# Optimization experiments

Hardware: AMD Instinct MI355X
Metric: run time of the kernel (lower is better)

## Reference

```python
import jax, jax.numpy as jnp
import numpy as np

B, T, D = 64, 256, 512   # batch, seq_len, input_dim (= emb_dim)
HA = 512                 # alpha_dim
HB = 512                 # beta_dim (must equal alpha_dim due to source bug)
ODE = 256                # ode_dim


def _lin(key, out_d, in_d, scale):
    k1, k2 = jax.random.split(key)
    W = jax.random.uniform(k1, (out_d, in_d), jnp.float32, -scale, scale)
    b = jax.random.uniform(k2, (out_d,), jnp.float32, -scale, scale)
    return W, b


def setup_inputs() -> dict:
    key = jax.random.key(0)
    ks = jax.random.split(key, 16)
    x = jax.random.normal(ks[0], (B, T, D), jnp.float32)
    W_emb, b_emb = _lin(ks[1], D, D, 1.0 / np.sqrt(D))
    # LSTMCell params: gates order i, f, g, o ; shapes (4H, in) / (4H, H)
    sA = 1.0 / np.sqrt(HA)
    Wih_a = jax.random.uniform(ks[2], (4 * HA, D), jnp.float32, -sA, sA)
    Whh_a = jax.random.uniform(ks[3], (4 * HA, HA), jnp.float32, -sA, sA)
    bih_a = jax.random.uniform(ks[4], (4 * HA,), jnp.float32, -sA, sA)
    bhh_a = jax.random.uniform(ks[5], (4 * HA,), jnp.float32, -sA, sA)
    sB = 1.0 / np.sqrt(HB)
    Wih_b = jax.random.uniform(ks[6], (4 * HB, D), jnp.float32, -sB, sB)
    Whh_b = jax.random.uniform(ks[7], (4 * HB, HB), jnp.float32, -sB, sB)
    bih_b = jax.random.uniform(ks[8], (4 * HB,), jnp.float32, -sB, sB)
    bhh_b = jax.random.uniform(ks[9], (4 * HB,), jnp.float32, -sB, sB)
    W_aatt, b_aatt = _lin(ks[10], 1, HA, 1.0 / np.sqrt(HA))
    W_batt, b_batt = _lin(ks[11], D, HB, 1.0 / np.sqrt(HB))
    W_mu, b_mu = _lin(ks[12], ODE, D, 1.0 / np.sqrt(D))
    W_sig, b_sig = _lin(ks[13], ODE, D, 1.0 / np.sqrt(D))
    ah0 = jax.random.normal(ks[14], (B, HA), jnp.float32)
    k15a, k15b, k15c = jax.random.split(ks[15], 3)
    ac0 = jax.random.normal(k15a, (B, HA), jnp.float32)
    bh0 = jax.random.normal(k15b, (B, HB), jnp.float32)
    bc0 = jax.random.normal(k15c, (B, HB), jnp.float32)
    return dict(x=x, W_emb=W_emb, b_emb=b_emb,
                Wih_a=Wih_a, Whh_a=Whh_a, bih_a=bih_a, bhh_a=bhh_a,
                Wih_b=Wih_b, Whh_b=Whh_b, bih_b=bih_b, bhh_b=bhh_b,
                W_aatt=W_aatt, b_aatt=b_aatt, W_batt=W_batt, b_batt=b_batt,
                W_mu=W_mu, b_mu=b_mu, W_sig=W_sig, b_sig=b_sig,
                ah0=ah0, ac0=ac0, bh0=bh0, bc0=bc0)


def _lstm_scan(xs, h0, c0, Wih, Whh, bih, bhh):
    # xs: (T, B, D) -> (hs (T,B,H), hT (B,H))
    def step(carry, xt):
        h, c = carry
        g = xt @ Wih.T + bih + h @ Whh.T + bhh
        i, f, gg, o = jnp.split(g, 4, axis=-1)
        c = jax.nn.sigmoid(f) * c + jax.nn.sigmoid(i) * jnp.tanh(gg)
        h = jax.nn.sigmoid(o) * jnp.tanh(c)
        return (h, c), h
    (hT, _), hs = jax.lax.scan(step, (h0, c0), xs)
    return hs, hT


def reference(x, W_emb, b_emb, Wih_a, Whh_a, bih_a, bhh_a,
              Wih_b, Whh_b, bih_b, bhh_b, W_aatt, b_aatt,
              W_batt, b_batt, W_mu, b_mu, W_sig, b_sig,
              ah0, ac0, bh0, bc0):
    emb = x @ W_emb.T + b_emb                      # (B, T, D)
    rev = jnp.flip(emb.transpose(1, 0, 2), 0)      # (T, B, D) reversed time
    hs_a, hT_a = _lstm_scan(rev, ah0, ac0, Wih_a, Whh_a, bih_a, bhh_a)
    hi = jnp.flip(hs_a, 0).transpose(1, 0, 2)      # (B, T, HA)
    alpha = jax.nn.softmax(hi @ W_aatt.T + b_aatt, axis=1)  # (B, T, 1)
    # Faithful to source bug: beta loop appends the FINAL alpha_hx each step,
    # so gi is hT_a broadcast over time (beta LSTM output is discarded).
    _ = _lstm_scan(rev, bh0, bc0, Wih_b, Whh_b, bih_b, bhh_b)  # dead compute, DCE'd
    gi = jnp.broadcast_to(hT_a[:, None, :], (x.shape[0], x.shape[1], hT_a.shape[-1]))
    beta = jnp.tanh(gi @ W_batt.T + b_batt)        # (B, T, D)
    w = alpha * beta * emb                          # (B, T, D)
    var = jnp.sum(w, axis=1)                        # (B, D)
    mean = jnp.mean(w, axis=1)                      # (B, D)
    mu = mean @ W_mu.T + b_mu                       # (B, ODE)
    sigma = var @ W_sig.T + b_sig                   # (B, ODE)
    return (mu, sigma)
```

## Files before the change

kernel.cpp:

```cpp
#include <hip/hip_runtime.h>
#include <hip/hip_bf16.h>
#include <math.h>

#define BB_ 64
#define TT_ 256
#define DD_ 512
#define HH_ 512
#define G4_ 2048
#define ODE_ 256

#define NBLK_ 256

__device__ __forceinline__ float2 cohload2(const float* p) {
    unsigned long long u = __hip_atomic_load(
        (unsigned long long*)p, __ATOMIC_RELAXED, __HIP_MEMORY_SCOPE_AGENT);
    union { unsigned long long u; float2 f; } c; c.u = u;
    return c.f;
}
__device__ __forceinline__ void cohstore2(float* p, float a, float b) {
    union { unsigned long long u; float2 f; } c; c.f = make_float2(a, b);
    __hip_atomic_store((unsigned long long*)p, c.u,
                       __ATOMIC_RELAXED, __HIP_MEMORY_SCOPE_AGENT);
}

__device__ __forceinline__ float fsigmoid(float x) {
    return 1.f / (1.f + __expf(-x));
}
__device__ __forceinline__ float ftanh(float x) {
    float e = __expf(-2.f * fabsf(x));
    float t = (1.f - e) / (1.f + e);
    return copysignf(t, x);
}

template <int CTRL>
__device__ __forceinline__ float dpp_ror_add(float x) {
    int y = __builtin_amdgcn_update_dpp(0, __float_as_int(x), CTRL, 0xf, 0xf, false);
    return x + __int_as_float(y);
}
__device__ __forceinline__ float row16_allreduce(float x) {
    x = dpp_ror_add<0x121>(x);
    x = dpp_ror_add<0x122>(x);
    x = dpp_ror_add<0x124>(x);
    x = dpp_ror_add<0x128>(x);
    return x;
}

template <int ACT>
__global__ __launch_bounds__(256) void gemm_bt(
    const float* __restrict__ A, const float* __restrict__ W,
    const float* __restrict__ bias1, const float* __restrict__ bias2,
    float* __restrict__ C, int M, int N, int K, float scale)
{
    const int BM = 128, BN = 128, BK = 16;
    __shared__ float As[BK][BM + 4];
    __shared__ float Ws[BK][BN + 4];
    const int tid = threadIdx.x;
    const int tx = tid & 15, ty = tid >> 4;
    const int m0 = blockIdx.y * BM, n0 = blockIdx.x * BN;

    float acc[8][8];
#pragma unroll
    for (int i = 0; i < 8; ++i)
#pragma unroll
        for (int j = 0; j < 8; ++j) acc[i][j] = 0.f;

    for (int k0 = 0; k0 < K; k0 += BK) {
#pragma unroll
        for (int i = 0; i < 2; ++i) {
            int lin = (i * 256 + tid) * 4;
            int r = lin >> 4, c = lin & 15;
            int gm = m0 + r; if (gm > M - 1) gm = M - 1;
            float4 av = *(const float4*)(A + (size_t)gm * K + k0 + c);
            As[c + 0][r] = av.x; As[c + 1][r] = av.y;
            As[c + 2][r] = av.z; As[c + 3][r] = av.w;
            float4 wv = *(const float4*)(W + (size_t)(n0 + r) * K + k0 + c);
            Ws[c + 0][r] = wv.x; Ws[c + 1][r] = wv.y;
            Ws[c + 2][r] = wv.z; Ws[c + 3][r] = wv.w;
        }
        __syncthreads();
#pragma unroll
        for (int k = 0; k < BK; ++k) {
            float a[8], w[8];
#pragma unroll
            for (int i = 0; i < 8; ++i) a[i] = As[k][ty * 8 + i];
#pragma unroll
            for (int j = 0; j < 8; ++j) w[j] = Ws[k][tx * 8 + j];
#pragma unroll
            for (int i = 0; i < 8; ++i)
#pragma unroll
                for (int j = 0; j < 8; ++j) acc[i][j] += a[i] * w[j];
        }
        __syncthreads();
    }

#pragma unroll
    for (int j = 0; j < 8; ++j) {
        int n = n0 + tx * 8 + j;
        float bsum = bias1[n] + (bias2 ? bias2[n] : 0.f);
#pragma unroll
        for (int i = 0; i < 8; ++i) {
            int m = m0 + ty * 8 + i;
            if (m < M) {
                float v = acc[i][j] * scale + bsum;
                if (ACT == 1) v = tanhf(v);
                C[(size_t)m * N + n] = v;
            }
        }
    }
}

__global__ __launch_bounds__(256) void lstm_persist(
    const float* __restrict__ gx,
    const float* __restrict__ Whh,
    const float* __restrict__ ac0,
    float* __restrict__ hT0,
    float* __restrict__ hT1,
    float* __restrict__ hsT,
    unsigned* __restrict__ cnt)
{
    __shared__ float h_s[512 * 20];
    __shared__ float gx_s[8 * 65];

    const int tid = threadIdx.x;
    const int jb = blockIdx.x >> 3;
    const int bg = blockIdx.x & 7;
    const int jh0 = jb * 16;
    const int b0  = bg * 8;
    const int kq   = tid & 15;
    const int jh_l = tid >> 4;
    const int jh   = jh0 + jh_l;

    float creg = 0.f;
    if (kq < 8) creg = ac0[(size_t)(b0 + kq) * HH_ + jh];

    float4 wreg[32];
#pragma unroll
    for (int kk = 0; kk < 32; ++kk) {
        int k = kk * 16 + kq;
        wreg[kk].x = Whh[(size_t)(0 * 512 + jh) * 512 + k];
        wreg[kk].y = Whh[(size_t)(1 * 512 + jh) * 512 + k];
        wreg[kk].z = Whh[(size_t)(2 * 512 + jh) * 512 + k];
        wreg[kk].w = Whh[(size_t)(3 * 512 + jh) * 512 + k];
    }

    const int g_lb  = tid >> 5;
    const int g_g   = (tid >> 3) & 3;
    const int g_jl2 = (tid & 7) * 2;
    const float* gsrc = gx + (size_t)(b0 + g_lb) * TT_ * G4_ + g_g * 512 + jh0 + g_jl2;

    float2 gxreg = *(const float2*)(gsrc + (size_t)255 * G4_);

    for (int t = 0; t < TT_; ++t) {
        const float* hin = ((t & 1) ? hT1 : hT0) + (size_t)bg * 4096;
        float* hout      = ((t & 1) ? hT0 : hT1) + (size_t)bg * 4096;

        gx_s[g_lb * 65 + g_g * 16 + g_jl2]     = gxreg.x;
        gx_s[g_lb * 65 + g_g * 16 + g_jl2 + 1] = gxreg.y;

        float4 hstg[4];
#pragma unroll
        for (int w = 0; w < 4; ++w) {
            int c = w * 256 + tid;
            float2 a  = cohload2(hin + (size_t)c * 4);
            float2 b2 = cohload2(hin + (size_t)c * 4 + 2);
            hstg[w] = make_float4(a.x, a.y, b2.x, b2.y);
        }
#pragma unroll
        for (int w = 0; w < 4; ++w) {
            int c = w * 256 + tid;
            *(float4*)(h_s + (c >> 1) * 20 + (c & 1) * 4) = hstg[w];
        }
        __syncthreads();

        if (t + 1 < TT_)
            gxreg = *(const float2*)(gsrc + (size_t)(TT_ - 2 - t) * G4_);

        float acc[8][4];
#pragma unroll
        for (int i = 0; i < 8; ++i)
#pragma unroll
            for (int j = 0; j < 4; ++j) acc[i][j] = 0.f;

#pragma unroll
        for (int kk = 0; kk < 32; ++kk) {
            int k = kk * 16 + kq;
            float4 wv = wreg[kk];
            float4 ha = *(const float4*)(h_s + (size_t)k * 20);
            float4 hb = *(const float4*)(h_s + (size_t)k * 20 + 4);
            float hv[8] = {ha.x, ha.y, ha.z, ha.w, hb.x, hb.y, hb.z, hb.w};
#pragma unroll
            for (int bb = 0; bb < 8; ++bb) {
                acc[bb][0] += hv[bb] * wv.x;
                acc[bb][1] += hv[bb] * wv.y;
                acc[bb][2] += hv[bb] * wv.z;
                acc[bb][3] += hv[bb] * wv.w;
            }
        }

#pragma unroll
        for (int bb = 0; bb < 8; ++bb)
#pragma unroll
            for (int g = 0; g < 4; ++g)
                acc[bb][g] = row16_allreduce(acc[bb][g]);

        float hn = 0.f;
        if (kq < 8) {
            float gi = 0.f, gf = 0.f, gg = 0.f, go = 0.f;
#pragma unroll
            for (int bb = 0; bb < 8; ++bb)
                if (kq == bb) { gi = acc[bb][0]; gf = acc[bb][1];
                                gg = acc[bb][2]; go = acc[bb][3]; }
            gi += gx_s[kq * 65 + 0 * 16 + jh_l];
            gf += gx_s[kq * 65 + 1 * 16 + jh_l];
            gg += gx_s[kq * 65 + 2 * 16 + jh_l];
            go += gx_s[kq * 65 + 3 * 16 + jh_l];
            float si = fsigmoid(gi);
            float sf = fsigmoid(gf);
            float sg = ftanh(gg);
            float so = fsigmoid(go);
            creg = sf * creg + si * sg;
            hn = so * ftanh(creg);
        }
        float hn_up = __shfl_down(hn, 1);
        const bool do_st = (kq < 8) && ((kq & 1) == 0);
        if (do_st)
            cohstore2(hout + (size_t)jh * 8 + kq, hn, hn_up);

        __syncthreads();
        if (tid == 0)
            __hip_atomic_fetch_add(&cnt[(size_t)bg * 32], 1u,
                                   __ATOMIC_RELAXED, __HIP_MEMORY_SCOPE_AGENT);
        if (do_st)
            *(float2*)(hsT + ((size_t)t * 512 + jh) * 64 + b0 + kq) = make_float2(hn, hn_up);
        if (tid == 0) {
            unsigned tgt = (unsigned)(t + 1) * 32u;
            while (__hip_atomic_load(&cnt[(size_t)bg * 32],
                        __ATOMIC_RELAXED, __HIP_MEMORY_SCOPE_AGENT) < tgt)
                __builtin_amdgcn_s_sleep(1);
        }
        __syncthreads();
    }
}

__global__ __launch_bounds__(256) void h0_transpose(
    const float* __restrict__ ah0, float* __restrict__ hT0)
{
    int idx = blockIdx.x * 256 + threadIdx.x;
    int b = idx >> 9, jh = idx & 511;
    hT0[(size_t)(b >> 3) * 4096 + jh * 8 + (b & 7)] = ah0[idx];
}

__global__ __launch_bounds__(256) void att_scores_T(
    const float* __restrict__ hsT, const float* __restrict__ Wa,
    const float* __restrict__ ba, float* __restrict__ scores)
{
    int ts = blockIdx.x;
    int b = threadIdx.x & 63, part = threadIdx.x >> 6;
    const float* hp = hsT + (size_t)ts * 512 * 64;
    float s = 0.f;
#pragma unroll 8
    for (int jj = 0; jj < 128; ++jj) {
        int jh = part * 128 + jj;
        s += hp[(size_t)jh * 64 + b] * Wa[jh];
    }
    __shared__ float red[4][64];
    red[part][b] = s;
    __syncthreads();
    if (part == 0) {
        float tot = red[0][b] + red[1][b] + red[2][b] + red[3][b] + ba[0];
        scores[b * TT_ + (TT_ - 1 - ts)] = tot;
    }
}

__global__ __launch_bounds__(256) void softmax_wsum(
    const float* __restrict__ scores, const float* __restrict__ emb,
    float* __restrict__ s)
{
    const int b = blockIdx.x;
    const int tid = threadIdx.x;
    __shared__ float sm[256];
    __shared__ float red[16];
    float v = scores[b * TT_ + tid];
    float m = v;
#pragma unroll
    for (int off = 32; off; off >>= 1) m = fmaxf(m, __shfl_xor(m, off));
    int wv = tid >> 6, ln = tid & 63;
    if (ln == 0) red[wv] = m;
    __syncthreads();
    float bm = fmaxf(fmaxf(red[0], red[1]), fmaxf(red[2], red[3]));
    float e = expf(v - bm);
    float ss = e;
#pragma unroll
    for (int off = 32; off; off >>= 1) ss += __shfl_xor(ss, off);
    if (ln == 0) red[8 + wv] = ss;
    __syncthreads();
    float tot = red[8] + red[9] + red[10] + red[11];
    sm[tid] = e / tot;
    __syncthreads();

    float acc0 = 0.f, acc1 = 0.f;
    const float* ep = emb + (size_t)b * TT_ * DD_;
    for (int t = 0; t < TT_; ++t) {
        float a = sm[t];
        acc0 += a * ep[t * DD_ + tid];
        acc1 += a * ep[t * DD_ + 256 + tid];
    }
    s[b * DD_ + tid] = acc0;
    s[b * DD_ + 256 + tid] = acc1;
}

__global__ __launch_bounds__(256) void beta_from_hT(
    const float* __restrict__ hTT, const float* __restrict__ Wb,
    const float* __restrict__ bbias, float* __restrict__ beta)
{
    int b = threadIdx.x & 63, w = threadIdx.x >> 6;
    int d = blockIdx.x * 4 + w;
    const float* wrow = Wb + (size_t)d * 512;
    const float* hb = hTT + (size_t)(b >> 3) * 4096 + (b & 7);
    float s = 0.f;
#pragma unroll 8
    for (int jh = 0; jh < 512; ++jh)
        s += hb[(size_t)jh * 8] * wrow[jh];
    beta[(size_t)b * 512 + d] = tanhf(s + bbias[d]);
}

__global__ __launch_bounds__(256) void mulvec(
    const float* __restrict__ a, const float* __restrict__ b,
    float* __restrict__ o, int n)
{
    int i = blockIdx.x * 256 + threadIdx.x;
    if (i < n) o[i] = a[i] * b[i];
}

extern "C" void kernel_launch(void* const* d_in, const int* in_sizes, int n_in,
                              void* d_out, int out_size, void* d_ws, size_t ws_size,
                              hipStream_t stream) {
    const float* x      = (const float*)d_in[0];
    const float* W_emb  = (const float*)d_in[1];
    const float* b_emb  = (const float*)d_in[2];
    const float* Wih_a  = (const float*)d_in[3];
    const float* Whh_a  = (const float*)d_in[4];
    const float* bih_a  = (const float*)d_in[5];
    const float* bhh_a  = (const float*)d_in[6];
    const float* W_aatt = (const float*)d_in[11];
    const float* b_aatt = (const float*)d_in[12];
    const float* W_batt = (const float*)d_in[13];
    const float* b_batt = (const float*)d_in[14];
    const float* W_mu   = (const float*)d_in[15];
    const float* b_mu   = (const float*)d_in[16];
    const float* W_sig  = (const float*)d_in[17];
    const float* b_sig  = (const float*)d_in[18];
    const float* ah0    = (const float*)d_in[19];
    const float* ac0    = (const float*)d_in[20];

    const size_t N_EMB = (size_t)BB_ * TT_ * DD_;
    const size_t N_GX  = (size_t)BB_ * TT_ * G4_;
    const size_t N_HS  = (size_t)TT_ * HH_ * BB_;
    const size_t N_BH  = (size_t)BB_ * HH_;
    const size_t N_BAR = 8192;

    size_t need_floats = N_BAR + N_EMB + N_GX + N_HS + 2 * N_BH
                       + (size_t)BB_ * TT_ + 3 * N_BH;
    if (ws_size < need_floats * sizeof(float)) return;

    float* ws     = (float*)d_ws;
    unsigned* cnt = (unsigned*)d_ws;
    float* emb    = ws + N_BAR;
    float* gx     = emb + N_EMB;
    float* hsT    = gx + N_GX;
    float* hT0    = hsT + N_HS;
    float* hT1    = hT0 + N_BH;
    float* scores = hT1 + N_BH;
    float* svec   = scores + (size_t)BB_ * TT_;
    float* beta   = svec + N_BH;
    float* var    = beta + N_BH;

    float* out_mu  = (float*)d_out;
    float* out_sig = out_mu + (size_t)BB_ * ODE_;

    hipMemsetAsync(d_ws, 0, N_BAR * sizeof(float), stream);

    h0_transpose<<<dim3(128), dim3(256), 0, stream>>>(ah0, hT0);

    gemm_bt<0><<<dim3(DD_ / 128, (BB_ * TT_) / 128), dim3(256), 0, stream>>>(
        x, W_emb, b_emb, nullptr, emb, BB_ * TT_, DD_, DD_, 1.f);

    gemm_bt<0><<<dim3(G4_ / 128, (BB_ * TT_) / 128), dim3(256), 0, stream>>>(
        emb, Wih_a, bih_a, bhh_a, gx, BB_ * TT_, G4_, DD_, 1.f);

    lstm_persist<<<dim3(NBLK_), dim3(256), 0, stream>>>(
        gx, Whh_a, ac0, hT0, hT1, hsT, cnt);

    att_scores_T<<<dim3(TT_), dim3(256), 0, stream>>>(hsT, W_aatt, b_aatt, scores);

    softmax_wsum<<<dim3(BB_), dim3(256), 0, stream>>>(scores, emb, svec);

    beta_from_hT<<<dim3(DD_ / 4), dim3(256), 0, stream>>>(hT0, W_batt, b_batt, beta);

    mulvec<<<dim3(N_BH / 256), dim3(256), 0, stream>>>(beta, svec, var, (int)N_BH);

    gemm_bt<0><<<dim3(ODE_ / 128, 1), dim3(256), 0, stream>>>(
        var, W_mu, b_mu, nullptr, out_mu, BB_, ODE_, DD_, 1.f / 256.f);
    gemm_bt<0><<<dim3(ODE_ / 128, 1), dim3(256), 0, stream>>>(
        var, W_sig, b_sig, nullptr, out_sig, BB_, ODE_, DD_, 1.f);
}
```

Measured before the change: 1.782 ms.

## Replace block-level barriers with per-wavefront counters in recurrent LSTM sync

The inter-block step barrier is rewritten so each wavefront signals its own counter slot after draining its stores, and every wavefront polls the four per-wave counters of its batch group itself. This removes two __syncthreads per timestep and the single-thread serialisation of the grid barrier. In exchange it relies on s_waitcnt ordering rather than block barriers for visibility of h stores, and the counter array is now four times larger. The last step skips the barrier entirely.

```diff
diff --git a/kernel.cpp b/kernel.cpp
--- a/kernel.cpp
+++ b/kernel.cpp
@@ -129,6 +129,8 @@
     const int kq   = tid & 15;
     const int jh_l = tid >> 4;
     const int jh   = jh0 + jh_l;
+    const int wv   = tid >> 6;
+    const int ln   = tid & 63;
 
     float creg = 0.f;
     if (kq < 8) creg = ac0[(size_t)(b0 + kq) * HH_ + jh];
@@ -184,16 +186,16 @@
 #pragma unroll
         for (int kk = 0; kk < 32; ++kk) {
             int k = kk * 16 + kq;
-            float4 wv = wreg[kk];
+            float4 wvv = wreg[kk];
             float4 ha = *(const float4*)(h_s + (size_t)k * 20);
             float4 hb = *(const float4*)(h_s + (size_t)k * 20 + 4);
             float hv[8] = {ha.x, ha.y, ha.z, ha.w, hb.x, hb.y, hb.z, hb.w};
 #pragma unroll
             for (int bb = 0; bb < 8; ++bb) {
-                acc[bb][0] += hv[bb] * wv.x;
-                acc[bb][1] += hv[bb] * wv.y;
-                acc[bb][2] += hv[bb] * wv.z;
-                acc[bb][3] += hv[bb] * wv.w;
+                acc[bb][0] += hv[bb] * wvv.x;
+                acc[bb][1] += hv[bb] * wvv.y;
+                acc[bb][2] += hv[bb] * wvv.z;
+                acc[bb][3] += hv[bb] * wvv.w;
             }
         }
 
@@ -226,19 +228,29 @@
         if (do_st)
             cohstore2(hout + (size_t)jh * 8 + kq, hn, hn_up);
 
-        __syncthreads();
-        if (tid == 0)
-            __hip_atomic_fetch_add(&cnt[(size_t)bg * 32], 1u,
-                                   __ATOMIC_RELAXED, __HIP_MEMORY_SCOPE_AGENT);
-        if (do_st)
-            *(float2*)(hsT + ((size_t)t * 512 + jh) * 64 + b0 + kq) = make_float2(hn, hn_up);
-        if (tid == 0) {
+        if (t + 1 < TT_) {
+            asm volatile("s_waitcnt vmcnt(0)" ::: "memory");
+            if (ln == 0)
+                __hip_atomic_fetch_add(&cnt[(size_t)(bg * 4 + wv) * 32], 1u,
+                                       __ATOMIC_RELAXED, __HIP_MEMORY_SCOPE_AGENT);
+            if (do_st)
+                *(float2*)(hsT + ((size_t)t * 512 + jh) * 64 + b0 + kq)
+                    = make_float2(hn, hn_up);
             unsigned tgt = (unsigned)(t + 1) * 32u;
-            while (__hip_atomic_load(&cnt[(size_t)bg * 32],
-                        __ATOMIC_RELAXED, __HIP_MEMORY_SCOPE_AGENT) < tgt)
+            for (;;) {
+                bool ok = true;
+                if (ln < 4)
+                    ok = __hip_atomic_load(&cnt[(size_t)(bg * 4 + ln) * 32],
+                             __ATOMIC_RELAXED, __HIP_MEMORY_SCOPE_AGENT) >= tgt;
+                if (__all(ok)) break;
                 __builtin_amdgcn_s_sleep(1);
-        }
-        __syncthreads();
+            }
+            asm volatile("" ::: "memory");
+        } else {
+            if (do_st)
+                *(float2*)(hsT + ((size_t)t * 512 + jh) * 64 + b0 + kq)
+                    = make_float2(hn, hn_up);
+        }
     }
 }
 
```

Measured after the change: 2.712 ms. 1.52x slower.
